# Optimization experiments

Hardware: AMD Instinct MI355X
Metric: run time of the kernel (lower is better)

Reference implementation:

```python
import jax, jax.numpy as jnp
import numpy as np

B, C, H, W = 8, 256, 64, 64
CM = C // 4          # mask channels (theta/phi out) = 64
CI = C - CM          # img channels = 192
EPS = 1e-5


def setup_inputs() -> dict:
    key = jax.random.key(0)
    ks = jax.random.split(key, 12)
    return {
        "x": jax.random.normal(ks[0], (B, C, H, W), dtype=jnp.float32),
        "g_w": jax.random.normal(ks[1], (C, C), dtype=jnp.float32) * 0.05,
        "g_b": jax.random.normal(ks[2], (C,), dtype=jnp.float32) * 0.01,
        "theta_w": jax.random.normal(ks[3], (CM, CM), dtype=jnp.float32) * 0.1,
        "theta_b": jax.random.normal(ks[4], (CM,), dtype=jnp.float32) * 0.01,
        "phi_w": jax.random.normal(ks[5], (CM, CI), dtype=jnp.float32) * 0.06,
        "phi_b": jax.random.normal(ks[6], (CM,), dtype=jnp.float32) * 0.01,
        "W_w": jax.random.normal(ks[7], (C, C), dtype=jnp.float32) * 0.05,
        "W_b": jax.random.normal(ks[8], (C,), dtype=jnp.float32) * 0.01,
        "bn_gamma": jax.random.normal(ks[9], (C,), dtype=jnp.float32) * 0.1 + 1.0,
        "bn_beta": jax.random.normal(ks[10], (C,), dtype=jnp.float32) * 0.01,
        "bn_mean": jax.random.normal(ks[11], (C,), dtype=jnp.float32) * 0.1,
        "bn_var": jnp.ones((C,), dtype=jnp.float32),
    }


def _conv1x1(t, w, b):
    # [B,Cin,H,W] x [Cout,Cin] -> [B,Cout,H,W]
    return jnp.einsum('bchw,oc->bohw', t, w) + b[None, :, None, None]


def _maxpool2(t):
    b, c, h, w = t.shape
    return t.reshape(b, c, h // 2, 2, w // 2, 2).max(axis=(3, 5))


def reference(x, g_w, g_b, theta_w, theta_b, phi_w, phi_b, W_w, W_b,
              bn_gamma, bn_beta, bn_mean, bn_var):
    b, c, h, w = x.shape
    ci = c // 4
    mask_ch = x[:, :ci]          # [B, C/4, H, W]
    img_ch = x[:, ci:]           # [B, 3C/4, H, W]

    # g: conv1x1 then 2x2 maxpool -> [B, C, N'] -> [B, N', C]
    g_x = _maxpool2(_conv1x1(x, g_w, g_b)).reshape(b, c, -1).transpose(0, 2, 1)
    # theta: conv1x1 on mask -> [B, N, C/4]
    theta_x = _conv1x1(mask_ch, theta_w, theta_b).reshape(b, ci, -1).transpose(0, 2, 1)
    # phi: conv1x1 on img then pool -> [B, C/4, N']
    phi_x = _maxpool2(_conv1x1(img_ch, phi_w, phi_b)).reshape(b, ci, -1)

    f = jnp.einsum('bnc,bcm->bnm', theta_x, phi_x)     # [B, N, N']
    f_div_C = jax.nn.softmax(f, axis=-1)
    y = jnp.einsum('bnm,bmc->bnc', f_div_C, g_x)       # [B, N, C]
    y = y.transpose(0, 2, 1).reshape(b, c, h, w)

    W_y = _conv1x1(y, W_w, W_b)
    # BatchNorm (inference form with running stats)
    inv = jax.lax.rsqrt(bn_var + EPS)
    W_y = (W_y - bn_mean[None, :, None, None]) * (inv * bn_gamma)[None, :, None, None] \
          + bn_beta[None, :, None, None]
    return W_y + x
```

## Files before the change

### kernel.cpp

```cpp
#include <hip/hip_runtime.h>
#include <hip/hip_bf16.h>

typedef __hip_bfloat16 bf16;
typedef unsigned short ushort;
typedef unsigned int uint;
typedef __attribute__((ext_vector_type(8))) short short8;
typedef __attribute__((ext_vector_type(4))) float f32x4;

#define Bn 8
#define Cn 256
#define Nn 4096
#define Mn 1024
#define EPSf 1e-5f

__device__ __forceinline__ float b2f(const bf16 v){ return __bfloat162float(v); }
__device__ __forceinline__ ushort f2bu(float f){
  uint u = __float_as_uint(f);
  return (ushort)((u + 0x7FFFu + ((u >> 16) & 1u)) >> 16);
}

__global__ __launch_bounds__(256) void transpose_kernel(
    const float* __restrict__ x, bf16* __restrict__ xT)
{
  __shared__ float xs[64][65];
  const int t = threadIdx.x;
  const int p0 = blockIdx.x*64, c0 = blockIdx.y*64, b = blockIdx.z;
  #pragma unroll
  for (int i = 0; i < 16; ++i) {
    int idx = t + i*256; int cl = idx >> 6, pl = idx & 63;
    xs[cl][pl] = x[((long)(b*Cn) + c0 + cl)*Nn + p0 + pl];
  }
  __syncthreads();
  ushort* xTu = (ushort*)xT;
  #pragma unroll
  for (int i = 0; i < 8; ++i) {
    int idx = t + i*256; int pl = idx >> 5, cp = idx & 31;
    uint u = (uint)f2bu(xs[cp*2][pl]) | ((uint)f2bu(xs[cp*2+1][pl]) << 16);
    *(uint*)(xTu + ((long)(b*Nn) + p0 + pl)*Cn + c0 + cp*2) = u;
  }
}

__global__ __launch_bounds__(256) void wcomb_kernel(
    const float* __restrict__ tw, const float* __restrict__ tb,
    const float* __restrict__ pw, const float* __restrict__ pb,
    const float* __restrict__ gw, const float* __restrict__ gb,
    bf16* __restrict__ Wcomb, float* __restrict__ bcomb)
{
  const int r = blockIdx.x, c = threadIdx.x;
  float v;
  if (r < 64)        v = (c < 64)  ? tw[r*64 + c]            : 0.f;
  else if (r < 128)  v = (c >= 64) ? pw[(r-64)*192 + (c-64)] : 0.f;
  else               v = gw[(r-128)*256 + c];
  Wcomb[r*256 + c] = __float2bfloat16(v);
  if (c == 0)
    bcomb[r] = (r < 64) ? tb[r] : (r < 128) ? pb[r-64] : gb[r-128];
}

__global__ __launch_bounds__(256) void gemm384_kernel(
    const bf16* __restrict__ xT, const bf16* __restrict__ Wcomb,
    const float* __restrict__ bcomb, bf16* __restrict__ Q,
    bf16* __restrict__ K, bf16* __restrict__ Vt)
{
  __shared__ union {
    struct { ushort As[128*40]; ushort Bs[128*40]; } g;
    float Pb[2][128][33];
  } sm;
  const int t = threadIdx.x;
  const int px = blockIdx.x, o0 = blockIdx.y*128, b = blockIdx.z;
  const int p0 = px*128;
  const int lane = t & 63, w = t >> 6;
  const int ql = lane & 15, quad = lane >> 4;
  const int wm = (w & 1)*64, wn = (w >> 1)*64;
  const ushort* xTu = (const ushort*)xT;
  const ushort* Wu  = (const ushort*)Wcomb;

  f32x4 acc[4][4];
  #pragma unroll
  for (int i = 0; i < 4; ++i)
    #pragma unroll
    for (int j = 0; j < 4; ++j) acc[i][j] = (f32x4){0.f,0.f,0.f,0.f};

  for (int kc = 0; kc < 8; ++kc) {
    __syncthreads();
    #pragma unroll
    for (int i = 0; i < 2; ++i) {
      int idx = t + i*256; int r = idx >> 2, cq = idx & 3;
      *(uint4*)(sm.g.As + r*40 + cq*8) =
          *(const uint4*)(xTu + ((long)(b*Nn) + p0 + r)*Cn + kc*32 + cq*8);
      *(uint4*)(sm.g.Bs + r*40 + cq*8) =
          *(const uint4*)(Wu + (o0 + r)*Cn + kc*32 + cq*8);
    }
    __syncthreads();
    short8 aF[4], bF[4];
    #pragma unroll
    for (int mi = 0; mi < 4; ++mi)
      aF[mi] = *(const short8*)(sm.g.As + (wm + mi*16 + ql)*40 + quad*8);
    #pragma unroll
    for (int ni = 0; ni < 4; ++ni)
      bF[ni] = *(const short8*)(sm.g.Bs + (wn + ni*16 + ql)*40 + quad*8);
    #pragma unroll
    for (int mi = 0; mi < 4; ++mi)
      #pragma unroll
      for (int ni = 0; ni < 4; ++ni)
        acc[mi][ni] = __builtin_amdgcn_mfma_f32_16x16x32_bf16(aF[mi], bF[ni], acc[mi][ni], 0, 0, 0);
  }
  float bias[4];
  #pragma unroll
  for (int ni = 0; ni < 4; ++ni) bias[ni] = bcomb[o0 + wn + ni*16 + ql];

  if (o0 == 0 && wn == 0) {
    #pragma unroll
    for (int mi = 0; mi < 4; ++mi)
      #pragma unroll
      for (int ni = 0; ni < 4; ++ni)
        #pragma unroll
        for (int r = 0; r < 4; ++r) {
          int p = p0 + wm + mi*16 + quad*4 + r;
          Q[((long)(b*Nn) + p)*64 + ni*16 + ql] = __float2bfloat16(acc[mi][ni][r] + bias[ni]);
        }
  }
  __syncthreads();
  if (o0 != 0 || wn == 64) {
    int g = w & 1;
    #pragma unroll
    for (int mi = 0; mi < 4; ++mi)
      #pragma unroll
      for (int ni = 0; ni < 4; ++ni) {
        float a0 = acc[mi][ni][0] + bias[ni], a1 = acc[mi][ni][1] + bias[ni];
        float a2 = acc[mi][ni][2] + bias[ni], a3 = acc[mi][ni][3] + bias[ni];
        int o = wn + ni*16 + ql;
        int wp = mi*8 + quad*2;
        sm.Pb[g][o][wp]     = fmaxf(a0, a1);
        sm.Pb[g][o][wp + 1] = fmaxf(a2, a3);
      }
  }
  __syncthreads();
  if (o0 == 0) {
    int wp = t & 31, og = t >> 5;
    ushort kv[8];
    #pragma unroll
    for (int j = 0; j < 8; ++j) {
      int o = 64 + og*8 + j;
      kv[j] = f2bu(fmaxf(sm.Pb[0][o][wp], sm.Pb[1][o][wp]));
    }
    *(uint4*)((ushort*)K + ((long)(b*Mn) + px*32 + wp)*64 + og*8) = *(uint4*)kv;
  } else {
    int ol = t >> 1, wp0 = (t & 1)*16;
    ushort vv[16];
    #pragma unroll
    for (int j = 0; j < 16; ++j)
      vv[j] = f2bu(fmaxf(sm.Pb[0][ol][wp0 + j], sm.Pb[1][ol][wp0 + j]));
    ushort* dst = (ushort*)Vt + ((long)(b*Cn) + (o0 - 128) + ol)*Mn + px*32 + wp0;
    *(uint4*)dst       = *(uint4*)(vv);
    *(uint4*)(dst + 8) = *(uint4*)(vv + 8);
  }
}

__global__ __launch_bounds__(512) void attn_kernel(
    const bf16* __restrict__ Q, const bf16* __restrict__ K, const bf16* __restrict__ Vt,
    bf16* __restrict__ Y)
{
  __shared__ __align__(16) ushort Ks[64*68];
  __shared__ __align__(16) ushort Vs[256*68];
  __shared__ __align__(16) ushort Ps[64*68];
  __shared__ float l_sh[2][64];

  const int t = threadIdx.x;
  const int b = blockIdx.y, q0 = blockIdx.x*64;
  const int lane = t & 63, w = t >> 6;
  const int ql = lane & 15, quad = lane >> 4;
  const int rt = w & 3;
  const int kh = w >> 2;
  const int rh = (w & 1)*32;
  const int cq = (w >> 1)*64;
  const ushort* Qu = (const ushort*)Q;
  const ushort* Ku = (const ushort*)K;
  const ushort* Vu = (const ushort*)Vt;

  const long qrow = (long)(b*Nn) + q0 + rt*16 + ql;
  short8 aQ0 = *(const short8*)(Qu + qrow*64 + quad*8);
  short8 aQ1 = *(const short8*)(Qu + qrow*64 + 32 + quad*8);

  float lrow[4];
  #pragma unroll
  for (int r = 0; r < 4; ++r) lrow[r] = 0.f;

  f32x4 acc[2][4];
  #pragma unroll
  for (int mi = 0; mi < 2; ++mi)
    #pragma unroll
    for (int ci = 0; ci < 4; ++ci) acc[mi][ci] = (f32x4){0.f,0.f,0.f,0.f};

  for (int mt = 0; mt < 16; ++mt) {
    const int m0 = mt*64;
    __syncthreads();
    {
      int ch = t & 7, rr = t >> 3;
      *(uint4*)(Ks + rr*68 + ch*8) =
          *(const uint4*)(Ku + ((long)(b*Mn) + m0 + rr)*64 + ch*8);
      #pragma unroll
      for (int p = 0; p < 4; ++p) {
        int n = rr + 64*p;
        *(uint4*)(Vs + n*68 + ch*8) =
            *(const uint4*)(Vu + ((long)(b*Cn) + n)*Mn + m0 + ch*8);
      }
    }
    __syncthreads();
    #pragma unroll
    for (int ct = 0; ct < 2; ++ct) {
      int kb = kh*32 + ct*16;
      short8 b0 = *(const short8*)(Ks + (kb + ql)*68 + quad*8);
      short8 b1 = *(const short8*)(Ks + (kb + ql)*68 + 32 + quad*8);
      f32x4 s = (f32x4){0.f,0.f,0.f,0.f};
      s = __builtin_amdgcn_mfma_f32_16x16x32_bf16(aQ0, b0, s, 0, 0, 0);
      s = __builtin_amdgcn_mfma_f32_16x16x32_bf16(aQ1, b1, s, 0, 0, 0);
      #pragma unroll
      for (int r = 0; r < 4; ++r) {
        float e = __expf(s[r]);
        lrow[r] += e;
        Ps[(rt*16 + quad*4 + r)*68 + kb + ql] = f2bu(e);
      }
    }
    __syncthreads();
    short8 aP0[2], aP1[2];
    #pragma unroll
    for (int mi = 0; mi < 2; ++mi) {
      aP0[mi] = *(const short8*)(Ps + (rh + mi*16 + ql)*68 + quad*8);
      aP1[mi] = *(const short8*)(Ps + (rh + mi*16 + ql)*68 + 32 + quad*8);
    }
    #pragma unroll
    for (int ci = 0; ci < 4; ++ci) {
      short8 b0 = *(const short8*)(Vs + (cq + ci*16 + ql)*68 + quad*8);
      short8 b1 = *(const short8*)(Vs + (cq + ci*16 + ql)*68 + 32 + quad*8);
      #pragma unroll
      for (int mi = 0; mi < 2; ++mi) {
        acc[mi][ci] = __builtin_amdgcn_mfma_f32_16x16x32_bf16(aP0[mi], b0, acc[mi][ci], 0, 0, 0);
        acc[mi][ci] = __builtin_amdgcn_mfma_f32_16x16x32_bf16(aP1[mi], b1, acc[mi][ci], 0, 0, 0);
      }
    }
  }
  #pragma unroll
  for (int r = 0; r < 4; ++r)
    #pragma unroll
    for (int off = 1; off < 16; off <<= 1)
      lrow[r] += __shfl_xor(lrow[r], off, 64);
  if (ql == 0) {
    #pragma unroll
    for (int r = 0; r < 4; ++r) l_sh[kh][rt*16 + quad*4 + r] = lrow[r];
  }
  __syncthreads();
  #pragma unroll
  for (int mi = 0; mi < 2; ++mi)
    #pragma unroll
    for (int r = 0; r < 4; ++r) {
      int row = rh + mi*16 + quad*4 + r;
      float inv = 1.f / (l_sh[0][row] + l_sh[1][row]);
      #pragma unroll
      for (int ci = 0; ci < 4; ++ci)
        Y[((long)(b*Nn) + q0 + row)*256 + cq + ci*16 + ql] = __float2bfloat16(acc[mi][ci][r]*inv);
    }
}

__global__ __launch_bounds__(256) void wconv_kernel(
    const bf16* __restrict__ Y, const float* __restrict__ Ww, const float* __restrict__ Wb,
    const float* __restrict__ gamma, const float* __restrict__ beta,
    const float* __restrict__ mean, const float* __restrict__ var,
    const float* __restrict__ x, float* __restrict__ out)
{
  __shared__ __align__(16) ushort As[128*40];
  __shared__ __align__(16) ushort Bs[128*40];
  __shared__ float ssc[128], ssh[128];
  const int t = threadIdx.x;
  const int n0 = blockIdx.x*128, o0 = blockIdx.y*128, b = blockIdx.z;
  const int lane = t & 63, w = t >> 6;
  const int ql = lane & 15, quad = lane >> 4;
  const int wm = (w & 1)*64, wn = (w >> 1)*64;
  const ushort* Yu = (const ushort*)Y;

  if (t < 128) {
    int o = o0 + t;
    float sc = gamma[o] * rsqrtf(var[o] + EPSf);
    ssc[t] = sc;
    ssh[t] = (Wb[o] - mean[o])*sc + beta[o];
  }

  f32x4 acc[4][4];
  #pragma unroll
  for (int i = 0; i < 4; ++i)
    #pragma unroll
    for (int j = 0; j < 4; ++j) acc[i][j] = (f32x4){0.f,0.f,0.f,0.f};

  for (int kc = 0; kc < 8; ++kc) {
    __syncthreads();
    #pragma unroll
    for (int i = 0; i < 4; ++i) {
      int idx = t + i*256; int r = idx >> 3, cq = idx & 7;
      float4 v = *(const float4*)(Ww + (o0 + r)*Cn + kc*32 + cq*4);
      uint lo = (uint)f2bu(v.x) | ((uint)f2bu(v.y) << 16);
      uint hi = (uint)f2bu(v.z) | ((uint)f2bu(v.w) << 16);
      *(uint2*)(As + r*40 + cq*4) = make_uint2(lo, hi);
    }
    #pragma unroll
    for (int i = 0; i < 2; ++i) {
      int idx = t + i*256; int r = idx >> 2, cq = idx & 3;
      *(uint4*)(Bs + r*40 + cq*8) =
          *(const uint4*)(Yu + ((long)(b*Nn) + n0 + r)*Cn + kc*32 + cq*8);
    }
    __syncthreads();
    short8 aF[4], bF[4];
    #pragma unroll
    for (int mi = 0; mi < 4; ++mi)
      aF[mi] = *(const short8*)(As + (wm + mi*16 + ql)*40 + quad*8);
    #pragma unroll
    for (int ni = 0; ni < 4; ++ni)
      bF[ni] = *(const short8*)(Bs + (wn + ni*16 + ql)*40 + quad*8);
    #pragma unroll
    for (int mi = 0; mi < 4; ++mi)
      #pragma unroll
      for (int ni = 0; ni < 4; ++ni)
        acc[mi][ni] = __builtin_amdgcn_mfma_f32_16x16x32_bf16(aF[mi], bF[ni], acc[mi][ni], 0, 0, 0);
  }
  #pragma unroll
  for (int mi = 0; mi < 4; ++mi)
    #pragma unroll
    for (int r = 0; r < 4; ++r) {
      int ol = wm + mi*16 + quad*4 + r;
      int o = o0 + ol;
      float sc = ssc[ol], sh = ssh[ol];
      #pragma unroll
      for (int ni = 0; ni < 4; ++ni) {
        int n = n0 + wn + ni*16 + ql;
        long gidx = ((long)(b*Cn + o))*Nn + n;
        out[gidx] = acc[mi][ni][r]*sc + sh + x[gidx];
      }
    }
}

extern "C" void kernel_launch(void* const* d_in, const int* in_sizes, int n_in,
                              void* d_out, int out_size, void* d_ws, size_t ws_size,
                              hipStream_t stream)
{
  const float* x       = (const float*)d_in[0];
  const float* g_w     = (const float*)d_in[1];
  const float* g_b     = (const float*)d_in[2];
  const float* theta_w = (const float*)d_in[3];
  const float* theta_b = (const float*)d_in[4];
  const float* phi_w   = (const float*)d_in[5];
  const float* phi_b   = (const float*)d_in[6];
  const float* W_w     = (const float*)d_in[7];
  const float* W_b     = (const float*)d_in[8];
  const float* bn_g    = (const float*)d_in[9];
  const float* bn_b    = (const float*)d_in[10];
  const float* bn_m    = (const float*)d_in[11];
  const float* bn_v    = (const float*)d_in[12];
  float* out = (float*)d_out;

  bf16* wsb = (bf16*)d_ws;
  bf16* xT    = wsb;
  bf16* Y     = wsb;
  bf16* Q     = wsb + 8388608;
  bf16* K     = wsb + 10485760;
  bf16* Vt    = wsb + 11010048;
  bf16* Wcomb = wsb + 13107200;
  float* bcomb = (float*)(wsb + 13205504);

  transpose_kernel<<<dim3(64, 4, Bn), 256, 0, stream>>>(x, xT);
  wcomb_kernel<<<dim3(384), 256, 0, stream>>>(theta_w, theta_b, phi_w, phi_b, g_w, g_b, Wcomb, bcomb);
  gemm384_kernel<<<dim3(32, 3, Bn), 256, 0, stream>>>(xT, Wcomb, bcomb, Q, K, Vt);
  attn_kernel<<<dim3(64, Bn), 512, 0, stream>>>(Q, K, Vt, Y);
  wconv_kernel<<<dim3(32, 2, Bn), 256, 0, stream>>>(Y, W_w, W_b, bn_g, bn_b, bn_m, bn_v, x, out);
}
```

Baseline: 185.1 us.

## Load K/V fragments directly from global into registers with prefetch, double-buffer P

The attention kernel stops staging K and V tiles through shared memory. Each wave now loads its MFMA operand fragments straight from global memory into registers, prefetching the next tile while computing the current one. The P tile is double-buffered so that each iteration needs one barrier instead of three. In exchange, K/V reads are duplicated across waves, which relies on L1/L2 for reuse, and the loads have narrower per-lane access patterns, while register pressure goes up.

Result: slower. 242.0 us (+30.7%).

```diff
diff --git a/kernel.cpp b/kernel.cpp
--- a/kernel.cpp
+++ b/kernel.cpp
@@ -160,9 +160,7 @@
     const bf16* __restrict__ Q, const bf16* __restrict__ K, const bf16* __restrict__ Vt,
     bf16* __restrict__ Y)
 {
-  __shared__ __align__(16) ushort Ks[64*68];
-  __shared__ __align__(16) ushort Vs[256*68];
-  __shared__ __align__(16) ushort Ps[64*68];
+  __shared__ __align__(16) ushort Ps[2][64*68];
   __shared__ float l_sh[2][64];
 
   const int t = threadIdx.x;
@@ -181,6 +179,9 @@
   short8 aQ0 = *(const short8*)(Qu + qrow*64 + quad*8);
   short8 aQ1 = *(const short8*)(Qu + qrow*64 + 32 + quad*8);
 
+  const ushort* kbase = Ku + ((long)(b*Mn) + kh*32 + ql)*64 + quad*8;
+  const ushort* vbase = Vu + ((long)(b*Cn) + cq + ql)*Mn + quad*8;
+
   float lrow[4];
   #pragma unroll
   for (int r = 0; r < 4; ++r) lrow[r] = 0.f;
@@ -191,53 +192,60 @@
     #pragma unroll
     for (int ci = 0; ci < 4; ++ci) acc[mi][ci] = (f32x4){0.f,0.f,0.f,0.f};
 
+  short8 kf[4], vf[8];
+  #pragma unroll
+  for (int ct = 0; ct < 2; ++ct) {
+    kf[ct*2]   = *(const short8*)(kbase + ct*16*64);
+    kf[ct*2+1] = *(const short8*)(kbase + ct*16*64 + 32);
+  }
+  #pragma unroll
+  for (int ci = 0; ci < 4; ++ci) {
+    vf[ci*2]   = *(const short8*)(vbase + ci*16*Mn);
+    vf[ci*2+1] = *(const short8*)(vbase + ci*16*Mn + 32);
+  }
+
+  int buf = 0;
   for (int mt = 0; mt < 16; ++mt) {
-    const int m0 = mt*64;
-    __syncthreads();
-    {
-      int ch = t & 7, rr = t >> 3;
-      *(uint4*)(Ks + rr*68 + ch*8) =
-          *(const uint4*)(Ku + ((long)(b*Mn) + m0 + rr)*64 + ch*8);
-      #pragma unroll
-      for (int p = 0; p < 4; ++p) {
-        int n = rr + 64*p;
-        *(uint4*)(Vs + n*68 + ch*8) =
-            *(const uint4*)(Vu + ((long)(b*Cn) + n)*Mn + m0 + ch*8);
-      }
-    }
-    __syncthreads();
+    const int m1 = ((mt + 1) & 15)*64;
     #pragma unroll
     for (int ct = 0; ct < 2; ++ct) {
       int kb = kh*32 + ct*16;
-      short8 b0 = *(const short8*)(Ks + (kb + ql)*68 + quad*8);
-      short8 b1 = *(const short8*)(Ks + (kb + ql)*68 + 32 + quad*8);
       f32x4 s = (f32x4){0.f,0.f,0.f,0.f};
-      s = __builtin_amdgcn_mfma_f32_16x16x32_bf16(aQ0, b0, s, 0, 0, 0);
-      s = __builtin_amdgcn_mfma_f32_16x16x32_bf16(aQ1, b1, s, 0, 0, 0);
+      s = __builtin_amdgcn_mfma_f32_16x16x32_bf16(aQ0, kf[ct*2],   s, 0, 0, 0);
+      s = __builtin_amdgcn_mfma_f32_16x16x32_bf16(aQ1, kf[ct*2+1], s, 0, 0, 0);
       #pragma unroll
       for (int r = 0; r < 4; ++r) {
         float e = __expf(s[r]);
         lrow[r] += e;
-        Ps[(rt*16 + quad*4 + r)*68 + kb + ql] = f2bu(e);
+        Ps[buf][(rt*16 + quad*4 + r)*68 + kb + ql] = f2bu(e);
       }
     }
+    #pragma unroll
+    for (int ct = 0; ct < 2; ++ct) {
+      kf[ct*2]   = *(const short8*)(kbase + (m1 + ct*16)*64);
+      kf[ct*2+1] = *(const short8*)(kbase + (m1 + ct*16)*64 + 32);
+    }
     __syncthreads();
     short8 aP0[2], aP1[2];
     #pragma unroll
     for (int mi = 0; mi < 2; ++mi) {
-      aP0[mi] = *(const short8*)(Ps + (rh + mi*16 + ql)*68 + quad*8);
-      aP1[mi] = *(const short8*)(Ps + (rh + mi*16 + ql)*68 + 32 + quad*8);
+      aP0[mi] = *(const short8*)(&Ps[buf][(rh + mi*16 + ql)*68 + quad*8]);
+      aP1[mi] = *(const short8*)(&Ps[buf][(rh + mi*16 + ql)*68 + 32 + quad*8]);
     }
     #pragma unroll
     for (int ci = 0; ci < 4; ++ci) {
-      short8 b0 = *(const short8*)(Vs + (cq + ci*16 + ql)*68 + quad*8);
-      short8 b1 = *(const short8*)(Vs + (cq + ci*16 + ql)*68 + 32 + quad*8);
       #pragma unroll
       for (int mi = 0; mi < 2; ++mi) {
-        acc[mi][ci] = __builtin_amdgcn_mfma_f32_16x16x32_bf16(aP0[mi], b0, acc[mi][ci], 0, 0, 0);
-        acc[mi][ci] = __builtin_amdgcn_mfma_f32_16x16x32_bf16(aP1[mi], b1, acc[mi][ci], 0, 0, 0);
+        acc[mi][ci] = __builtin_amdgcn_mfma_f32_16x16x32_bf16(aP0[mi], vf[ci*2],   acc[mi][ci], 0, 0, 0);
+        acc[mi][ci] = __builtin_amdgcn_mfma_f32_16x16x32_bf16(aP1[mi], vf[ci*2+1], acc[mi][ci], 0, 0, 0);
       }
     }
+    #pragma unroll
+    for (int ci = 0; ci < 4; ++ci) {
+      vf[ci*2]   = *(const short8*)(vbase + ci*16*Mn + m1);
+      vf[ci*2+1] = *(const short8*)(vbase + ci*16*Mn + m1 + 32);
+    }
+    buf ^= 1;
   }
   #pragma unroll
   for (int r = 0; r < 4; ++r)
```
